# Optimization experiments

Measured on AMD Instinct MI355X. Metric: run time of the kernel, lower is better.

The kernel has to match this reference:

```python
import jax, jax.numpy as jnp
import numpy as np

INPUT_DIM = 64
HIDDEN_DIM = 32


def setup_inputs() -> dict:
    key = jax.random.key(0)
    ks = jax.random.split(key, 9)
    B, C, H, W = 8, INPUT_DIM, 64, 64
    s_in = 1.0 / np.sqrt(C)
    inp = {
        "h": jax.random.normal(ks[0], (B, C, H, W), dtype=jnp.float32),
        # 1x1 conv weights stored as [out, in]
        "wq": jax.random.uniform(ks[1], (HIDDEN_DIM, C), jnp.float32, -s_in, s_in),
        "bq": jax.random.uniform(ks[2], (HIDDEN_DIM,), jnp.float32, -s_in, s_in),
        "wk": jax.random.uniform(ks[3], (HIDDEN_DIM, C), jnp.float32, -s_in, s_in),
        "bk": jax.random.uniform(ks[4], (HIDDEN_DIM,), jnp.float32, -s_in, s_in),
        "wv": jax.random.uniform(ks[5], (C, C), jnp.float32, -s_in, s_in),
        "bv": jax.random.uniform(ks[6], (C,), jnp.float32, -s_in, s_in),
        "wz": jax.random.uniform(ks[7], (C, C), jnp.float32, -s_in, s_in),
        "bz": jax.random.uniform(ks[8], (C,), jnp.float32, -s_in, s_in),
    }
    return inp


def reference(h, wq, bq, wk, bk, wv, bv, wz, bz):
    B, C, H, W = h.shape
    N = H * W
    x = h.reshape(B, C, N)  # [B, C, N]
    # 1x1 convs == channel-wise linear maps
    q = jnp.einsum('oc,bcn->bno', wq, x) + bq          # [B, N, Dh]
    k = jnp.einsum('oc,bcn->bon', wk, x) + bk[:, None]  # [B, Dh, N]
    v = jnp.einsum('oc,bcn->bon', wv, x) + bv[:, None]  # [B, C, N]
    attn = jax.nn.softmax(jnp.einsum('bnd,bdm->bnm', q, k), axis=-1)  # [B, N, N]
    z = jnp.einsum('bnm,bcm->bcn', attn, v)             # [B, C, N]
    out = jnp.einsum('oc,bcn->bon', wz, z) + bz[:, None]
    return out.reshape(B, C, H, W) + h
```

## Files before the change

### kernel.cpp

```cpp
#include <hip/hip_runtime.h>
#include <stdint.h>

#define BATCH 8
#define CIN   64
#define DH    32
#define NTOK  4096
#define LOG2E 1.4426950408889634f

typedef float    f4   __attribute__((ext_vector_type(4)));
typedef short    s8v  __attribute__((ext_vector_type(8)));
typedef uint32_t u32;
typedef uint32_t u32x2 __attribute__((ext_vector_type(2)));
typedef uint32_t u32x4 __attribute__((ext_vector_type(4)));

static __device__ __forceinline__ short f2bf(float f) {
    union { float f; u32 u; } c; c.f = f;
    u32 u = c.u;
    u32 r = (u + 0x7fffu + ((u >> 16) & 1u)) >> 16;
    return (short)(r & 0xffffu);
}
static __device__ __forceinline__ u32 pk2(float a, float b) {
    return (u32)(uint16_t)f2bf(a) | ((u32)(uint16_t)f2bf(b) << 16);
}
static __device__ __forceinline__ u32 pktr(float a, float b) {
    union { float f; u32 u; } ca, cb; ca.f = a; cb.f = b;
#if __has_builtin(__builtin_amdgcn_perm)
    return __builtin_amdgcn_perm(cb.u, ca.u, 0x07060302u);
#else
    return (cb.u & 0xffff0000u) | (ca.u >> 16);
#endif
}
static __device__ __forceinline__ float bfhi(u32 u) {
    union { u32 u; float f; } c; c.u = u & 0xffff0000u; return c.f;
}
static __device__ __forceinline__ float bflo(u32 u) {
    union { u32 u; float f; } c; c.u = u << 16; return c.f;
}

__global__ __launch_bounds__(256) void proj_kernel(
    const float* __restrict__ h,
    const float* __restrict__ wq, const float* __restrict__ bq,
    const float* __restrict__ wk, const float* __restrict__ bk,
    const float* __restrict__ wv, const float* __restrict__ bv,
    short* __restrict__ qbf, short* __restrict__ kbf, short* __restrict__ vp)
{
    __shared__ short xT [64 * 72];
    __shared__ short wqs[32 * 72];
    __shared__ short wks[32 * 72];
    __shared__ short wvs[64 * 72];
    __shared__ float bqs[32], bks[32], bvs[64];

    const int t   = threadIdx.x;
    const int b   = blockIdx.x;
    const int nt0 = blockIdx.y * 64;

    {
        const int c  = t >> 2;
        const int ng = (t & 3) * 16;
        const float* src = h + ((size_t)(b * CIN + c)) * NTOK + nt0 + ng;
        f4 x0 = *(const f4*)(src + 0);
        f4 x1 = *(const f4*)(src + 4);
        f4 x2 = *(const f4*)(src + 8);
        f4 x3 = *(const f4*)(src + 12);
        #pragma unroll
        for (int i = 0; i < 4; ++i) {
            xT[(ng + 0  + i) * 72 + c] = f2bf(x0[i]);
            xT[(ng + 4  + i) * 72 + c] = f2bf(x1[i]);
            xT[(ng + 8  + i) * 72 + c] = f2bf(x2[i]);
            xT[(ng + 12 + i) * 72 + c] = f2bf(x3[i]);
        }
    }
    for (int idx = t; idx < 2048; idx += 256) {
        int o = idx >> 6, c = idx & 63;
        wqs[o * 72 + c] = f2bf(wq[idx] * LOG2E);
        wks[o * 72 + c] = f2bf(wk[idx]);
    }
    for (int idx = t; idx < 4096; idx += 256)
        wvs[(idx >> 6) * 72 + (idx & 63)] = f2bf(wv[idx]);
    if (t < 32) { bqs[t] = bq[t] * LOG2E; bks[t] = bk[t]; }
    if (t < 64) bvs[t] = bv[t];
    __syncthreads();

    const int w    = t >> 6;
    const int ln   = t & 15;
    const int quad = (t >> 4) & 3;
    const int n    = nt0 + w * 16 + ln;
    const f4 zf4 = {0.f, 0.f, 0.f, 0.f};

    const s8v xb0 = *(const s8v*)&xT[(w * 16 + ln) * 72 + quad * 8];
    const s8v xb1 = *(const s8v*)&xT[(w * 16 + ln) * 72 + 32 + quad * 8];

    #pragma unroll
    for (int ot = 0; ot < 2; ++ot) {
        s8v a0 = *(const s8v*)&wqs[(ot * 16 + ln) * 72 + quad * 8];
        s8v a1 = *(const s8v*)&wqs[(ot * 16 + ln) * 72 + 32 + quad * 8];
        f4 d = __builtin_amdgcn_mfma_f32_16x16x32_bf16(a0, xb0, zf4, 0, 0, 0);
        d     = __builtin_amdgcn_mfma_f32_16x16x32_bf16(a1, xb1, d,  0, 0, 0);
        f4 bb = *(const f4*)&bqs[ot * 16 + quad * 4];
        u32x2 pw; pw[0] = pk2(d[0] + bb[0], d[1] + bb[1]);
                  pw[1] = pk2(d[2] + bb[2], d[3] + bb[3]);
        *(u32x2*)(qbf + ((size_t)(b * NTOK + n)) * DH + ot * 16 + quad * 4) = pw;

        s8v c0 = *(const s8v*)&wks[(ot * 16 + ln) * 72 + quad * 8];
        s8v c1 = *(const s8v*)&wks[(ot * 16 + ln) * 72 + 32 + quad * 8];
        f4 e = __builtin_amdgcn_mfma_f32_16x16x32_bf16(c0, xb0, zf4, 0, 0, 0);
        e     = __builtin_amdgcn_mfma_f32_16x16x32_bf16(c1, xb1, e,  0, 0, 0);
        f4 kb = *(const f4*)&bks[ot * 16 + quad * 4];
        u32x2 kw; kw[0] = pk2(e[0] + kb[0], e[1] + kb[1]);
                  kw[1] = pk2(e[2] + kb[2], e[3] + kb[3]);
        *(u32x2*)(kbf + ((size_t)(b * NTOK + n)) * DH + ot * 16 + quad * 4) = kw;
    }

    {
        const int cidx = n >> 5, p = n & 31;
        const int tt = p >> 4, qq = (p >> 2) & 3, r0 = p & 3;
        const int j = tt * 4 + r0;
        short* vdst = vp + ((size_t)((b * 128 + cidx) * 4 + qq) * 64) * 8 + j;
        #pragma unroll
        for (int ot = 0; ot < 4; ++ot) {
            s8v a0 = *(const s8v*)&wvs[(ot * 16 + ln) * 72 + quad * 8];
            s8v a1 = *(const s8v*)&wvs[(ot * 16 + ln) * 72 + 32 + quad * 8];
            f4 d = __builtin_amdgcn_mfma_f32_16x16x32_bf16(a0, xb0, zf4, 0, 0, 0);
            d     = __builtin_amdgcn_mfma_f32_16x16x32_bf16(a1, xb1, d,  0, 0, 0);
            #pragma unroll
            for (int r = 0; r < 4; ++r) {
                int ch = ot * 16 + quad * 4 + r;
                vdst[ch * 8] = f2bf(d[r] + bvs[ch]);
            }
        }
    }
}

__global__ __launch_bounds__(512, 2) void attn_kernel(
    const float* __restrict__ h,  const float* __restrict__ wz,
    const float* __restrict__ bz,
    const short* __restrict__ qbf, const short* __restrict__ kbf,
    const short* __restrict__ vp,  float* __restrict__ out)
{
    __shared__ short accb[4][64][72];
    __shared__ short zbuf[128][72];
    __shared__ float lbuf[8][64];

    const int b    = blockIdx.x;
    const int qb0  = blockIdx.y * 128;
    const int tid  = threadIdx.x;
    const int w    = tid >> 6;
    const int lane = tid & 63;
    const int ln   = lane & 15;
    const int quad = lane >> 4;
    const int qh   = w >> 2;
    const int ksec = w & 3;
    const int nbase = qb0 + qh * 64;
    const f4 zf4 = {0.f, 0.f, 0.f, 0.f};

    s8v qf[4];
    #pragma unroll
    for (int f = 0; f < 4; ++f)
        qf[f] = *(const s8v*)(qbf + ((size_t)(b * NTOK + nbase + f * 16 + ln)) * DH + quad * 8);

    f4 acc[4][4];
    f4 accl[4];
    #pragma unroll
    for (int f = 0; f < 4; ++f) {
        accl[f] = zf4;
        #pragma unroll
        for (int ct = 0; ct < 4; ++ct) acc[f][ct] = zf4;
    }
    s8v ones;
    #pragma unroll
    for (int j = 0; j < 8; ++j) ones[j] = (short)0x3F80;

    const short* kb = kbf + (size_t)b * NTOK * DH;
    const s8v*   vb = (const s8v*)(vp + (size_t)b * NTOK * CIN);

    const int kend = ksec * 1024 + 1024;
    for (int kt = ksec * 1024; kt < kend; kt += 32) {
        s8v kk0 = *(const s8v*)(kb + (kt + ln) * DH + quad * 8);
        s8v kk1 = *(const s8v*)(kb + (kt + 16 + ln) * DH + quad * 8);
        const s8v* vg = vb + (size_t)((kt >> 5) * 4 + quad) * 64 + ln;
        s8v v0 = vg[0], v1 = vg[16], v2 = vg[32], v3 = vg[48];

        #pragma unroll
        for (int f = 0; f < 4; ++f) {
            f4 sa = __builtin_amdgcn_mfma_f32_16x16x32_bf16(kk0, qf[f], zf4, 0, 0, 0);
            f4 sb = __builtin_amdgcn_mfma_f32_16x16x32_bf16(kk1, qf[f], zf4, 0, 0, 0);
            f4 ea, eb;
            #pragma unroll
            for (int r = 0; r < 4; ++r) {
                ea[r] = __builtin_amdgcn_exp2f(sa[r]);
                eb[r] = __builtin_amdgcn_exp2f(sb[r]);
            }
            u32x4 pd;
            pd[0] = pktr(ea[0], ea[1]); pd[1] = pktr(ea[2], ea[3]);
            pd[2] = pktr(eb[0], eb[1]); pd[3] = pktr(eb[2], eb[3]);
            s8v pf = __builtin_bit_cast(s8v, pd);

            accl[f]   = __builtin_amdgcn_mfma_f32_16x16x32_bf16(ones, pf, accl[f],   0, 0, 0);
            acc[f][0] = __builtin_amdgcn_mfma_f32_16x16x32_bf16(v0,   pf, acc[f][0], 0, 0, 0);
            acc[f][1] = __builtin_amdgcn_mfma_f32_16x16x32_bf16(v1,   pf, acc[f][1], 0, 0, 0);
            acc[f][2] = __builtin_amdgcn_mfma_f32_16x16x32_bf16(v2,   pf, acc[f][2], 0, 0, 0);
            acc[f][3] = __builtin_amdgcn_mfma_f32_16x16x32_bf16(v3,   pf, acc[f][3], 0, 0, 0);
        }
    }

    if (quad == 0) {
        #pragma unroll
        for (int f = 0; f < 4; ++f) lbuf[w][f * 16 + ln] = accl[f][0];
    }
    #define WRITE_SLOT(slot)                                                        \
        {                                                                           \
            _Pragma("unroll")                                                       \
            for (int f = 0; f < 4; ++f) {                                           \
                _Pragma("unroll")                                                   \
                for (int ct = 0; ct < 4; ++ct) {                                    \
                    u32x2 pw;                                                       \
                    pw[0] = pk2(acc[f][ct][0], acc[f][ct][1]);                      \
                    pw[1] = pk2(acc[f][ct][2], acc[f][ct][3]);                      \
                    *(u32x2*)&accb[slot][f * 16 + ln][ct * 16 + quad * 4] = pw;     \
                }                                                                   \
            }                                                                       \
        }
    if (w < 4) WRITE_SLOT(w);
    __syncthreads();

    #define COMBINE(half)                                                           \
        if (tid < 256) {                                                            \
            const int q   = tid >> 2;                                               \
            const int chg = (tid & 3) * 16;                                         \
            float ls = lbuf[(half) * 4 + 0][q] + lbuf[(half) * 4 + 1][q] +          \
                       lbuf[(half) * 4 + 2][q] + lbuf[(half) * 4 + 3][q];           \
            float rl = __builtin_amdgcn_rcpf(ls);                                   \
            float zv[16];                                                           \
            _Pragma("unroll")                                                       \
            for (int i = 0; i < 16; ++i) zv[i] = 0.f;                               \
            _Pragma("unroll")                                                       \
            for (int w2 = 0; w2 < 4; ++w2) {                                        \
                u32x4 ua = *(u32x4*)&accb[w2][q][chg];                              \
                u32x4 ub = *(u32x4*)&accb[w2][q][chg + 8];                          \
                _Pragma("unroll")                                                   \
                for (int d = 0; d < 4; ++d) {                                       \
                    zv[d * 2]     += bflo(ua[d]); zv[d * 2 + 1]     += bfhi(ua[d]); \
                    zv[8 + d * 2] += bflo(ub[d]); zv[8 + d * 2 + 1] += bfhi(ub[d]); \
                }                                                                   \
            }                                                                       \
            u32x4 za, zb2;                                                          \
            _Pragma("unroll")                                                       \
            for (int d = 0; d < 4; ++d) {                                           \
                za[d]  = pk2(zv[d * 2] * rl,     zv[d * 2 + 1] * rl);               \
                zb2[d] = pk2(zv[8 + d * 2] * rl, zv[8 + d * 2 + 1] * rl);           \
            }                                                                       \
            *(u32x4*)&zbuf[(half) * 64 + q][chg]     = za;                          \
            *(u32x4*)&zbuf[(half) * 64 + q][chg + 8] = zb2;                         \
        }
    COMBINE(0);
    __syncthreads();
    if (w >= 4) WRITE_SLOT(w - 4);
    __syncthreads();
    COMBINE(1);
    __syncthreads();

    {
        const int ot = w & 3, g = w >> 2;
        s8v wzf[2];
        #pragma unroll
        for (int half = 0; half < 2; ++half) {
            const float* wp = wz + (ot * 16 + ln) * 64 + half * 32 + quad * 8;
            f4 wa = *(const f4*)wp;
            f4 wb = *(const f4*)(wp + 4);
            u32x4 tt;
            tt[0] = pk2(wa[0], wa[1]); tt[1] = pk2(wa[2], wa[3]);
            tt[2] = pk2(wb[0], wb[1]); tt[3] = pk2(wb[2], wb[3]);
            wzf[half] = __builtin_bit_cast(s8v, tt);
        }
        f4 bzv = *(const f4*)(bz + ot * 16 + quad * 4);
        #pragma unroll
        for (int fi = 0; fi < 4; ++fi) {
            const int row = g * 64 + fi * 16 + ln;
            s8v z0 = *(const s8v*)&zbuf[row][quad * 8];
            s8v z1 = *(const s8v*)&zbuf[row][32 + quad * 8];
            f4 oa = __builtin_amdgcn_mfma_f32_16x16x32_bf16(wzf[0], z0, zf4, 0, 0, 0);
            oa     = __builtin_amdgcn_mfma_f32_16x16x32_bf16(wzf[1], z1, oa,  0, 0, 0);
            #pragma unroll
            for (int r = 0; r < 4; ++r) {
                size_t idx = ((size_t)(b * CIN + ot * 16 + quad * 4 + r)) * NTOK
                           + qb0 + row;
                out[idx] = oa[r] + bzv[r] + h[idx];
            }
        }
    }
}

extern "C" void kernel_launch(void* const* d_in, const int* in_sizes, int n_in,
                              void* d_out, int out_size, void* d_ws, size_t ws_size,
                              hipStream_t stream) {
    (void)in_sizes; (void)n_in; (void)out_size; (void)ws_size;
    const float* h  = (const float*)d_in[0];
    const float* wq = (const float*)d_in[1];
    const float* bq = (const float*)d_in[2];
    const float* wk = (const float*)d_in[3];
    const float* bk = (const float*)d_in[4];
    const float* wv = (const float*)d_in[5];
    const float* bv = (const float*)d_in[6];
    const float* wz = (const float*)d_in[7];
    const float* bz = (const float*)d_in[8];
    float* out = (float*)d_out;

    short* qbf = (short*)d_ws;
    short* kbf = qbf + (size_t)BATCH * NTOK * DH;
    short* vpw = kbf + (size_t)BATCH * NTOK * DH;

    proj_kernel<<<dim3(8, 64), dim3(256), 0, stream>>>(
        h, wq, bq, wk, bk, wv, bv, qbf, kbf, vpw);
    attn_kernel<<<dim3(8, 32), dim3(512), 0, stream>>>(
        h, wz, bz, qbf, kbf, vpw, out);
}
```

Measured before the change: 117.3 us.

## Stage V through LDS for coalesced stores and shrink attention blocks to 64 queries

The projection kernel now writes V tiles into a shared-memory staging buffer and then emits them as coalesced 16-byte global stores, replacing the scattered 2-byte stores. The attention kernel moves from 512-thread blocks covering 128 queries to 256-thread blocks covering 64 queries, with each of 4 waves owning a quarter of the keys. This doubles the grid to 512 blocks and removes the two-phase combine with its extra barriers. The trade-off is that each K/V tile is now reloaded by twice as many blocks.

New measurement: 115.7 us. About the same (-1.4%).

```diff
diff --git a/kernel.cpp b/kernel.cpp
--- a/kernel.cpp
+++ b/kernel.cpp
@@ -48,6 +48,7 @@
     __shared__ short wqs[32 * 72];
     __shared__ short wks[32 * 72];
     __shared__ short wvs[64 * 72];
+    __shared__ short vls2[64 * 68];
     __shared__ float bqs[32], bks[32], bvs[64];
 
     const int t   = threadIdx.x;
@@ -84,11 +85,12 @@
     const int w    = t >> 6;
     const int ln   = t & 15;
     const int quad = (t >> 4) & 3;
-    const int n    = nt0 + w * 16 + ln;
+    const int nl   = w * 16 + ln;
+    const int n    = nt0 + nl;
     const f4 zf4 = {0.f, 0.f, 0.f, 0.f};
 
-    const s8v xb0 = *(const s8v*)&xT[(w * 16 + ln) * 72 + quad * 8];
-    const s8v xb1 = *(const s8v*)&xT[(w * 16 + ln) * 72 + 32 + quad * 8];
+    const s8v xb0 = *(const s8v*)&xT[nl * 72 + quad * 8];
+    const s8v xb1 = *(const s8v*)&xT[nl * 72 + 32 + quad * 8];
 
     #pragma unroll
     for (int ot = 0; ot < 2; ++ot) {
@@ -112,51 +114,64 @@
     }
 
     {
-        const int cidx = n >> 5, p = n & 31;
-        const int tt = p >> 4, qq = (p >> 2) & 3, r0 = p & 3;
-        const int j = tt * 4 + r0;
-        short* vdst = vp + ((size_t)((b * 128 + cidx) * 4 + qq) * 64) * 8 + j;
+        const int p    = nl & 31;
+        const int row  = (nl >> 5) * 32 + ((p >> 2) & 3) * 8
+                       + (p >> 4) * 4 + (p & 3);
+        short* vrow = &vls2[row * 68];
         #pragma unroll
         for (int ot = 0; ot < 4; ++ot) {
             s8v a0 = *(const s8v*)&wvs[(ot * 16 + ln) * 72 + quad * 8];
             s8v a1 = *(const s8v*)&wvs[(ot * 16 + ln) * 72 + 32 + quad * 8];
             f4 d = __builtin_amdgcn_mfma_f32_16x16x32_bf16(a0, xb0, zf4, 0, 0, 0);
             d     = __builtin_amdgcn_mfma_f32_16x16x32_bf16(a1, xb1, d,  0, 0, 0);
+            const int ch = ot * 16 + quad * 4;
+            u32x2 pw;
+            pw[0] = pk2(d[0] + bvs[ch],     d[1] + bvs[ch + 1]);
+            pw[1] = pk2(d[2] + bvs[ch + 2], d[3] + bvs[ch + 3]);
+            *(u32x2*)&vrow[ch] = pw;
+        }
+    }
+    __syncthreads();
+
+    {
+        const int g = t >> 5;
+        const int r = t & 31;
+        short tmp[16];
+        #pragma unroll
+        for (int j = 0; j < 8; ++j)
             #pragma unroll
-            for (int r = 0; r < 4; ++r) {
-                int ch = ot * 16 + quad * 4 + r;
-                vdst[ch * 8] = f2bf(d[r] + bvs[ch]);
-            }
-        }
-    }
-}
-
-__global__ __launch_bounds__(512, 2) void attn_kernel(
+            for (int cc = 0; cc < 2; ++cc)
+                tmp[cc * 8 + j] = vls2[(g * 8 + j) * 68 + r * 2 + cc];
+        u32x4* dst = (u32x4*)(vp + ((size_t)(b * 128 + blockIdx.y * 2) * 4) * 64 * 8);
+        #pragma unroll
+        for (int i = 0; i < 2; ++i)
+            dst[t * 2 + i] = ((const u32x4*)tmp)[i];
+    }
+}
+
+__global__ __launch_bounds__(256, 2) void attn_kernel(
     const float* __restrict__ h,  const float* __restrict__ wz,
     const float* __restrict__ bz,
     const short* __restrict__ qbf, const short* __restrict__ kbf,
     const short* __restrict__ vp,  float* __restrict__ out)
 {
     __shared__ short accb[4][64][72];
-    __shared__ short zbuf[128][72];
-    __shared__ float lbuf[8][64];
+    __shared__ short zbuf[64][72];
+    __shared__ float lbuf[4][64];
 
     const int b    = blockIdx.x;
-    const int qb0  = blockIdx.y * 128;
+    const int qb0  = blockIdx.y * 64;
     const int tid  = threadIdx.x;
     const int w    = tid >> 6;
     const int lane = tid & 63;
     const int ln   = lane & 15;
     const int quad = lane >> 4;
-    const int qh   = w >> 2;
-    const int ksec = w & 3;
-    const int nbase = qb0 + qh * 64;
     const f4 zf4 = {0.f, 0.f, 0.f, 0.f};
 
     s8v qf[4];
     #pragma unroll
     for (int f = 0; f < 4; ++f)
-        qf[f] = *(const s8v*)(qbf + ((size_t)(b * NTOK + nbase + f * 16 + ln)) * DH + quad * 8);
+        qf[f] = *(const s8v*)(qbf + ((size_t)(b * NTOK + qb0 + f * 16 + ln)) * DH + quad * 8);
 
     f4 acc[4][4];
     f4 accl[4];
@@ -170,14 +185,15 @@
     #pragma unroll
     for (int j = 0; j < 8; ++j) ones[j] = (short)0x3F80;
 
-    const short* kb = kbf + (size_t)b * NTOK * DH;
-    const s8v*   vb = (const s8v*)(vp + (size_t)b * NTOK * CIN);
-
-    const int kend = ksec * 1024 + 1024;
-    for (int kt = ksec * 1024; kt < kend; kt += 32) {
-        s8v kk0 = *(const s8v*)(kb + (kt + ln) * DH + quad * 8);
-        s8v kk1 = *(const s8v*)(kb + (kt + 16 + ln) * DH + quad * 8);
-        const s8v* vg = vb + (size_t)((kt >> 5) * 4 + quad) * 64 + ln;
+    const short* kb2 = kbf + ((size_t)b * NTOK + w * 1024) * DH;
+    const s8v*   vb2 = (const s8v*)(vp + (size_t)b * NTOK * CIN)
+                     + (size_t)(w * 32) * 4 * 64;
+
+    for (int kt = 0; kt < 1024; kt += 32) {
+        const short* kp = kb2 + kt * DH;
+        s8v kk0 = *(const s8v*)(kp + ln * DH + quad * 8);
+        s8v kk1 = *(const s8v*)(kp + (16 + ln) * DH + quad * 8);
+        const s8v* vg = vb2 + (size_t)((kt >> 5) * 4 + quad) * 64 + ln;
         s8v v0 = vg[0], v1 = vg[16], v2 = vg[32], v3 = vg[48];
 
         #pragma unroll
@@ -207,60 +223,49 @@
         #pragma unroll
         for (int f = 0; f < 4; ++f) lbuf[w][f * 16 + ln] = accl[f][0];
     }
-    #define WRITE_SLOT(slot)                                                        \
-        {                                                                           \
-            _Pragma("unroll")                                                       \
-            for (int f = 0; f < 4; ++f) {                                           \
-                _Pragma("unroll")                                                   \
-                for (int ct = 0; ct < 4; ++ct) {                                    \
-                    u32x2 pw;                                                       \
-                    pw[0] = pk2(acc[f][ct][0], acc[f][ct][1]);                      \
-                    pw[1] = pk2(acc[f][ct][2], acc[f][ct][3]);                      \
-                    *(u32x2*)&accb[slot][f * 16 + ln][ct * 16 + quad * 4] = pw;     \
-                }                                                                   \
-            }                                                                       \
-        }
-    if (w < 4) WRITE_SLOT(w);
+    #pragma unroll
+    for (int f = 0; f < 4; ++f) {
+        #pragma unroll
+        for (int ct = 0; ct < 4; ++ct) {
+            u32x2 pw;
+            pw[0] = pk2(acc[f][ct][0], acc[f][ct][1]);
+            pw[1] = pk2(acc[f][ct][2], acc[f][ct][3]);
+            *(u32x2*)&accb[w][f * 16 + ln][ct * 16 + quad * 4] = pw;
+        }
+    }
     __syncthreads();
 
-    #define COMBINE(half)                                                           \
-        if (tid < 256) {                                                            \
-            const int q   = tid >> 2;                                               \
-            const int chg = (tid & 3) * 16;                                         \
-            float ls = lbuf[(half) * 4 + 0][q] + lbuf[(half) * 4 + 1][q] +          \
-                       lbuf[(half) * 4 + 2][q] + lbuf[(half) * 4 + 3][q];           \
-            float rl = __builtin_amdgcn_rcpf(ls);                                   \
-            float zv[16];                                                           \
-            _Pragma("unroll")                                                       \
-            for (int i = 0; i < 16; ++i) zv[i] = 0.f;                               \
-            _Pragma("unroll")                                                       \
-            for (int w2 = 0; w2 < 4; ++w2) {                                        \
-                u32x4 ua = *(u32x4*)&accb[w2][q][chg];                              \
-                u32x4 ub = *(u32x4*)&accb[w2][q][chg + 8];                          \
-                _Pragma("unroll")                                                   \
-                for (int d = 0; d < 4; ++d) {                                       \
-                    zv[d * 2]     += bflo(ua[d]); zv[d * 2 + 1]     += bfhi(ua[d]); \
-                    zv[8 + d * 2] += bflo(ub[d]); zv[8 + d * 2 + 1] += bfhi(ub[d]); \
-                }                                                                   \
-            }                                                                       \
-            u32x4 za, zb2;                                                          \
-            _Pragma("unroll")                                                       \
-            for (int d = 0; d < 4; ++d) {                                           \
-                za[d]  = pk2(zv[d * 2] * rl,     zv[d * 2 + 1] * rl);               \
-                zb2[d] = pk2(zv[8 + d * 2] * rl, zv[8 + d * 2 + 1] * rl);           \
-            }                                                                       \
-            *(u32x4*)&zbuf[(half) * 64 + q][chg]     = za;                          \
-            *(u32x4*)&zbuf[(half) * 64 + q][chg + 8] = zb2;                         \
-        }
-    COMBINE(0);
+    {
+        const int q   = tid >> 2;
+        const int chg = (tid & 3) * 16;
+        float ls = lbuf[0][q] + lbuf[1][q] + lbuf[2][q] + lbuf[3][q];
+        float rl = __builtin_amdgcn_rcpf(ls);
+        float zv[16];
+        #pragma unroll
+        for (int i = 0; i < 16; ++i) zv[i] = 0.f;
+        #pragma unroll
+        for (int w2 = 0; w2 < 4; ++w2) {
+            u32x4 ua = *(u32x4*)&accb[w2][q][chg];
+            u32x4 ub = *(u32x4*)&accb[w2][q][chg + 8];
+            #pragma unroll
+            for (int d = 0; d < 4; ++d) {
+                zv[d * 2]     += bflo(ua[d]); zv[d * 2 + 1]     += bfhi(ua[d]);
+                zv[8 + d * 2] += bflo(ub[d]); zv[8 + d * 2 + 1] += bfhi(ub[d]);
+            }
+        }
+        u32x4 za, zb2;
+        #pragma unroll
+        for (int d = 0; d < 4; ++d) {
+            za[d]  = pk2(zv[d * 2] * rl,     zv[d * 2 + 1] * rl);
+            zb2[d] = pk2(zv[8 + d * 2] * rl, zv[8 + d * 2 + 1] * rl);
+        }
+        *(u32x4*)&zbuf[q][chg]     = za;
+        *(u32x4*)&zbuf[q][chg + 8] = zb2;
+    }
     __syncthreads();
-    if (w >= 4) WRITE_SLOT(w - 4);
-    __syncthreads();
-    COMBINE(1);
-    __syncthreads();
-
-    {
-        const int ot = w & 3, g = w >> 2;
+
+    {
+        const int ot = w;
         s8v wzf[2];
         #pragma unroll
         for (int half = 0; half < 2; ++half) {
@@ -275,7 +280,7 @@
         f4 bzv = *(const f4*)(bz + ot * 16 + quad * 4);
         #pragma unroll
         for (int fi = 0; fi < 4; ++fi) {
-            const int row = g * 64 + fi * 16 + ln;
+            const int row = fi * 16 + ln;
             s8v z0 = *(const s8v*)&zbuf[row][quad * 8];
             s8v z1 = *(const s8v*)&zbuf[row][32 + quad * 8];
             f4 oa = __builtin_amdgcn_mfma_f32_16x16x32_bf16(wzf[0], z0, zf4, 0, 0, 0);
@@ -311,6 +316,6 @@
 
     proj_kernel<<<dim3(8, 64), dim3(256), 0, stream>>>(
         h, wq, bq, wk, bk, wv, bv, qbf, kbf, vpw);
-    attn_kernel<<<dim3(8, 32), dim3(512), 0, stream>>>(
+    attn_kernel<<<dim3(8, 64), dim3(256), 0, stream>>>(
         h, wz, bz, qbf, kbf, vpw, out);
 }
```
